# Kernel optimization log

Measured on AMD Instinct MI355X. Metric: run time of the kernel, lower is better.

The kernel has to match this reference:

```python
import jax, jax.numpy as jnp
import numpy as np

ALPHA = 0.2          # LeakyReLU slope
NEG_BIG = -9e15      # mask value from the torch code
LN_EPS = 1e-5        # torch LayerNorm default eps
GAT_SCALE = 1.0


def _layer_norm(x, g, b):
    mu = x.mean(-1, keepdims=True)
    var = ((x - mu) ** 2).mean(-1, keepdims=True)
    return (x - mu) * jax.lax.rsqrt(var + LN_EPS) * g + b


def _gat_layer(h, adj, W, a, concat):
    # h: [B,N,Fin], adj: [N,N] weighted, W: [Fin,Fout], a: [2*Fout,1]
    Wh = jnp.einsum('bnf,fo->bno', h, W)                 # [B,N,Fout]
    Fo = W.shape[1]
    a_i, a_j = a[:Fo, 0], a[Fo:, 0]
    # e[b,i,j] = leakyrelu(Wh[b,i].a_i + Wh[b,j].a_j)  (== cat([Wh_i,Wh_j]) @ a)
    e = jax.nn.leaky_relu(
        (Wh @ a_i)[:, :, None] + (Wh @ a_j)[:, None, :], ALPHA)  # [B,N,N]
    att = jnp.where(adj[None, :, :] > 0, e, NEG_BIG)
    att = jax.nn.softmax(att, axis=2)
    att = att * adj[None, :, :]
    att = att / (att.sum(axis=2, keepdims=True) + 1e-8)
    h_prime = jnp.einsum('bij,bjo->bio', att, Wh)        # [B,N,Fout]
    return jax.nn.elu(h_prime) if concat else h_prime


def setup_inputs() -> dict:
    B, N, H, ID = 1024, 128, 64, 8
    GIN = 1 + ID  # node_feat_dim = 0
    key = jax.random.key(0)
    ks = jax.random.split(key, 20)
    # sparse weighted adjacency with self-loops
    w = jax.random.uniform(ks[0], (N, N))
    m = (jax.random.uniform(ks[1], (N, N)) < 0.3).astype(jnp.float32)
    adj = w * m + jnp.eye(N, dtype=jnp.float32)
    sc = lambda k, s: jax.random.normal(k, s, jnp.float32) * 0.1
    return {
        'c_values': jax.random.normal(ks[2], (B, N), jnp.float32),
        'adj': adj,
        'agent_emb': sc(ks[3], (N, ID)),
        'W1': sc(ks[4], (GIN, H)), 'a1': sc(ks[5], (2 * H, 1)),
        'W2': sc(ks[6], (H, H)),   'a2': sc(ks[7], (2 * H, 1)),
        'ln1_g': jnp.ones((H,)), 'ln1_b': jnp.zeros((H,)),
        'ln2_g': jnp.ones((H,)), 'ln2_b': jnp.zeros((H,)),
        'head_gat_w': sc(ks[8], (H, 1)), 'head_gat_b': jnp.zeros((1,)),
        'mlp1_w': sc(ks[9], (N, H)),  'mlp1_b': jnp.zeros((H,)),
        'mlp2_w': sc(ks[10], (H, H)), 'mlp2_b': jnp.zeros((H,)),
        'head_mlp_w': sc(ks[11], (H, 1)), 'head_mlp_b': jnp.zeros((1,)),
        'gate1_w': sc(ks[12], (N, H)), 'gate1_b': jnp.zeros((H,)),
        'gate2_w': sc(ks[13], (H, 1)), 'gate2_b': jnp.full((1,), -5.0),
    }


def reference(c_values, adj, agent_emb, W1, a1, W2, a2,
              ln1_g, ln1_b, ln2_g, ln2_b, head_gat_w, head_gat_b,
              mlp1_w, mlp1_b, mlp2_w, mlp2_b, head_mlp_w, head_mlp_b,
              gate1_w, gate1_b, gate2_w, gate2_b):
    B, N = c_values.shape
    # node features: [c_value, agent_id_embedding]
    id_feat = jnp.broadcast_to(agent_emb[None], (B, N, agent_emb.shape[1]))
    x_g = jnp.concatenate([c_values[..., None], id_feat], axis=-1)  # [B,N,9]
    h1 = _gat_layer(x_g, adj, W1, a1, concat=True)
    h1 = _layer_norm(h1, ln1_g, ln1_b)
    h2 = _gat_layer(h1, adj, W2, a2, concat=False)
    h = jax.nn.relu(h2 + h1)
    h = _layer_norm(h, ln2_g, ln2_b)
    q_gat = h.mean(axis=1) @ head_gat_w + head_gat_b                # [B,1]
    x_m = jax.nn.relu(c_values @ mlp1_w + mlp1_b)
    x_m = jax.nn.relu(x_m @ mlp2_w + mlp2_b)
    q_mlp = x_m @ head_mlp_w + head_mlp_b                           # [B,1]
    gate = jax.nn.sigmoid(
        jax.nn.relu(c_values @ gate1_w + gate1_b) @ gate2_w + gate2_b)
    return q_mlp + gate * GAT_SCALE * q_gat
```

## Files before the change

kernel.cpp:

```cpp
#include <hip/hip_runtime.h>

typedef unsigned short u16;
typedef unsigned int u32;
typedef short v8s __attribute__((ext_vector_type(8)));
typedef float v4f __attribute__((ext_vector_type(4)));
typedef float v2f __attribute__((ext_vector_type(2)));

__device__ __forceinline__ float bflo(u32 d){union{u32 i;float f;}u;u.i=d<<16;return u.f;}
__device__ __forceinline__ float bfhi(u32 d){union{u32 i;float f;}u;u.i=d&0xffff0000u;return u.f;}
__device__ __forceinline__ u16 f2bfr(float f){union{float f;u32 i;}u;u.f=f;return (u16)((u.i+0x8000u)>>16);}
__device__ __forceinline__ u32 pk2bf(float a,float b){
    union{float f;u32 i;}ua,ub; ua.f=a; ub.f=b;
    u32 x = ua.i + 0x8000u, y = ub.i + 0x8000u;
    return __builtin_amdgcn_perm(y, x, 0x07060302);
}
__device__ __forceinline__ v8s pack8(const float* w){
    union { uint4 u; v8s v; } c;
    c.u.x = pk2bf(w[0],w[1]); c.u.y = pk2bf(w[2],w[3]);
    c.u.z = pk2bf(w[4],w[5]); c.u.w = pk2bf(w[6],w[7]);
    return c.v;
}

__device__ __forceinline__ void flash_att(
    int wv, int l15, int q4,
    const float* __restrict__ ADJ,
    const float* __restrict__ sEi, const float* __restrict__ sFi,
    const float* __restrict__ sEj, const float* __restrict__ sFj,
    const u16* __restrict__ sWhT,
    v4f acc[2][4], float invD[2])
{
    const int r0 = 16*wv + l15, r1 = r0 + 64;
    const v2f Ei0 = {sEi[r0], sEi[r0]}, Fi0 = {sFi[r0], sFi[r0]};
    const v2f Ei1 = {sEi[r1], sEi[r1]}, Fi1 = {sFi[r1], sFi[r1]};
    v2f D0 = {0.f,0.f}, D1 = {0.f,0.f};
    #pragma unroll
    for (int s = 0; s < 2; ++s)
        #pragma unroll
        for (int ct = 0; ct < 4; ++ct) acc[s][ct] = (v4f){0.f,0.f,0.f,0.f};

    #pragma unroll
    for (int ks = 0; ks < 4; ++ks) {
        const int ko = ks*32 + q4*8;
        const v2f* Ejp = (const v2f*)(sEj + ko);
        const v2f* Fjp = (const v2f*)(sFj + ko);
        const v2f* A0p = (const v2f*)(ADJ + r0*128 + ko);
        const v2f* A1p = (const v2f*)(ADJ + r1*128 + ko);
        union { u32 u[4]; v8s v; } P0, P1;
        #pragma unroll
        for (int p = 0; p < 4; ++p) {
            v2f E = Ejp[p], F = Fjp[p];
            v2f a0 = A0p[p], a1 = A1p[p];
            v2f m0 = __builtin_elementwise_max(Ei0*E, Fi0*F);
            v2f m1 = __builtin_elementwise_max(Ei1*E, Fi1*F);
            v2f x0 = m0 * a0;
            v2f x1 = m1 * a1;
            D0 += x0; D1 += x1;
            P0.u[p] = pk2bf(x0.x, x0.y);
            P1.u[p] = pk2bf(x1.x, x1.y);
        }
        #pragma unroll
        for (int ct = 0; ct < 4; ++ct) {
            v8s B = *(const v8s*)(sWhT + (16*ct + l15)*136 + ko);
            acc[0][ct] = __builtin_amdgcn_mfma_f32_16x16x32_bf16(P0.v, B, acc[0][ct], 0,0,0);
            acc[1][ct] = __builtin_amdgcn_mfma_f32_16x16x32_bf16(P1.v, B, acc[1][ct], 0,0,0);
        }
    }
    float d0 = D0.x + D0.y, d1 = D1.x + D1.y;
    d0 += __shfl_xor(d0, 16); d0 += __shfl_xor(d0, 32);
    d1 += __shfl_xor(d1, 16); d1 += __shfl_xor(d1, 32);
    invD[0] = 1.f / d0; invD[1] = 1.f / d1;
}

__global__ __launch_bounds__(256, 4) void graphmixer_kernel(
    const float* __restrict__ C,
    const float* __restrict__ ADJ,
    const float* __restrict__ EMB,
    const float* __restrict__ W1,
    const float* __restrict__ A1,
    const float* __restrict__ W2,
    const float* __restrict__ A2,
    const float* __restrict__ LN1G, const float* __restrict__ LN1B,
    const float* __restrict__ LN2G, const float* __restrict__ LN2B,
    const float* __restrict__ HGW,  const float* __restrict__ HGB,
    const float* __restrict__ MLP1W, const float* __restrict__ MLP1B,
    const float* __restrict__ MLP2W, const float* __restrict__ MLP2B,
    const float* __restrict__ HMW,  const float* __restrict__ HMB,
    const float* __restrict__ G1W,  const float* __restrict__ G1B,
    const float* __restrict__ G2W,  const float* __restrict__ G2B,
    float* __restrict__ OUT)
{
    const int b = blockIdx.x, t = threadIdx.x;
    const int lane = t & 63, wv = t >> 6;
    const int l15 = lane & 15, q4 = lane >> 4;

    __shared__ __align__(16) unsigned char smem[40096];
    u16*   sWhT = (u16*)(smem);
    u16*   sH1  = (u16*)(smem + 17408);
    float* sEi  = (float*)(smem + 35840);
    float* sFi  = (float*)(smem + 36352);
    float* sEj  = (float*)(smem + 36864);
    float* sFj  = (float*)(smem + 37376);
    float* colp = (float*)(smem + 37888);
    float* sScr = (float*)(smem + 38912);
    float* v2i  = (float*)(smem + 39456);
    float* v2j  = (float*)(smem + 39712);
    float* v1i  = (float*)(smem + 39968);
    float* v1j  = (float*)(smem + 40032);
    float* sEmb = (float*)(smem + 17408);
    float* sC   = (float*)(smem + 21504);

    const float* Cb = C + b*128;

    if (wv == 0) {
        #pragma unroll
        for (int q = 0; q < 4; ++q)
            ((float4*)sEmb)[lane + 64*q] = ((const float4*)EMB)[lane + 64*q];
        if (lane < 32) ((float4*)sC)[lane] = ((const float4*)Cb)[lane];
        if (lane >= 32 && lane < 41) {
            int f = lane - 32; float a = 0.f;
            for (int q = 0; q < 16; ++q) {
                float4 w = *(const float4*)(W1 + f*64 + q*4);
                float4 x = *(const float4*)(A1 + q*4);
                a += w.x*x.x + w.y*x.y + w.z*x.z + w.w*x.w;
            }
            v1i[f] = a;
        } else if (lane >= 48 && lane < 57) {
            int f = lane - 48; float a = 0.f;
            for (int q = 0; q < 16; ++q) {
                float4 w = *(const float4*)(W1 + f*64 + q*4);
                float4 x = *(const float4*)(A1 + 64 + q*4);
                a += w.x*x.x + w.y*x.y + w.z*x.z + w.w*x.w;
            }
            v1j[f] = a;
        }
    } else if (wv == 3) {
        float ai = 0.f, aj = 0.f;
        for (int q = 0; q < 16; ++q) {
            float4 w  = *(const float4*)(W2 + lane*64 + q*4);
            float4 xi = *(const float4*)(A2 + q*4);
            float4 xj = *(const float4*)(A2 + 64 + q*4);
            ai += w.x*xi.x + w.y*xi.y + w.z*xi.z + w.w*xi.w;
            aj += w.x*xj.x + w.y*xj.y + w.z*xj.z + w.w*xj.w;
        }
        v2i[lane] = ai; v2j[lane] = aj;
    } else if (wv == 1) {
        float a = 0.f;
        for (int k = 0; k < 128; k += 4) {
            float4 c4 = *(const float4*)(Cb + k);
            a += c4.x*MLP1W[k*64+lane] + c4.y*MLP1W[(k+1)*64+lane]
               + c4.z*MLP1W[(k+2)*64+lane] + c4.w*MLP1W[(k+3)*64+lane];
        }
        sScr[lane] = fmaxf(a + MLP1B[lane], 0.f);
        float a2 = 0.f;
        for (int k = 0; k < 64; ++k) a2 += sScr[k] * MLP2W[k*64 + lane];
        float x2 = fmaxf(a2 + MLP2B[lane], 0.f);
        float p1 = x2 * HMW[lane];
        #pragma unroll
        for (int off = 32; off >= 1; off >>= 1) p1 += __shfl_down(p1, off);
        if (lane == 0) sScr[128] = p1 + HMB[0];
    } else {
        float a = 0.f;
        for (int k = 0; k < 128; k += 4) {
            float4 c4 = *(const float4*)(Cb + k);
            a += c4.x*G1W[k*64+lane] + c4.y*G1W[(k+1)*64+lane]
               + c4.z*G1W[(k+2)*64+lane] + c4.w*G1W[(k+3)*64+lane];
        }
        float g1 = fmaxf(a + G1B[lane], 0.f);
        float p2 = g1 * G2W[lane];
        #pragma unroll
        for (int off = 32; off >= 1; off >>= 1) p2 += __shfl_down(p2, off);
        if (lane == 0) sScr[129] = 1.f / (1.f + __expf(-(p2 + G2B[0])));
    }
    __syncthreads();

    {
        v8s Af[2];
        #pragma unroll
        for (int s = 0; s < 2; ++s) {
            const int row = 16*(wv + 4*s) + l15;
            float av[8];
            #pragma unroll
            for (int j = 0; j < 8; ++j) av[j] = 0.f;
            if (q4 == 0) {
                av[0] = sC[row];
                float4 e0 = *(const float4*)(sEmb + row*8);
                float4 e1 = *(const float4*)(sEmb + row*8 + 4);
                av[1]=e0.x; av[2]=e0.y; av[3]=e0.z; av[4]=e0.w;
                av[5]=e1.x; av[6]=e1.y; av[7]=e1.z;
            } else if (q4 == 1) {
                av[0] = sEmb[row*8 + 7];
            }
            Af[s] = pack8(av);
        }
        #pragma unroll
        for (int ct = 0; ct < 4; ++ct) {
            const int col = 16*ct + l15;
            float bv[8];
            #pragma unroll
            for (int j = 0; j < 8; ++j) bv[j] = 0.f;
            if (q4 == 0) {
                #pragma unroll
                for (int j = 0; j < 8; ++j) bv[j] = W1[j*64 + col];
            } else if (q4 == 1) {
                bv[0] = W1[8*64 + col];
            }
            v8s Bf1 = pack8(bv);
            v4f a0 = (v4f){0.f,0.f,0.f,0.f}, a1 = (v4f){0.f,0.f,0.f,0.f};
            a0 = __builtin_amdgcn_mfma_f32_16x16x32_bf16(Af[0], Bf1, a0, 0,0,0);
            a1 = __builtin_amdgcn_mfma_f32_16x16x32_bf16(Af[1], Bf1, a1, 0,0,0);
            uint2 p0, p1;
            p0.x = pk2bf(a0[0], a0[1]); p0.y = pk2bf(a0[2], a0[3]);
            p1.x = pk2bf(a1[0], a1[1]); p1.y = pk2bf(a1[2], a1[3]);
            *(uint2*)(sWhT + col*136 + 16*wv      + 4*q4) = p0;
            *(uint2*)(sWhT + col*136 + 16*(wv+4)  + 4*q4) = p1;
        }
    }
    {
        const int row = t >> 1;
        const float* vv = (t & 1) ? v1j : v1i;
        float c = sC[row];
        float4 e0 = *(const float4*)(sEmb + row*8);
        float4 e1 = *(const float4*)(sEmb + row*8 + 4);
        float e = c*vv[0] + e0.x*vv[1]+e0.y*vv[2]+e0.z*vv[3]+e0.w*vv[4]
                          + e1.x*vv[5]+e1.y*vv[6]+e1.z*vv[7]+e1.w*vv[8];
        if (t & 1) { sEj[row] = __expf(e); sFj[row] = __expf(0.2f*e); }
        else       { sEi[row] = __expf(e); sFi[row] = __expf(0.2f*e); }
    }
    __syncthreads();

    {
        v4f acc[2][4]; float invD[2];
        flash_att(wv, l15, q4, ADJ, sEi, sFi, sEj, sFj, sWhT, acc, invD);

        float g4[4], b4[4];
        #pragma unroll
        for (int ct = 0; ct < 4; ++ct) { g4[ct] = LN1G[16*ct + l15]; b4[ct] = LN1B[16*ct + l15]; }
        #pragma unroll
        for (int s = 0; s < 2; ++s) {
            const int rbase = 16*(wv + 4*s) + 4*q4;
            #pragma unroll
            for (int reg = 0; reg < 4; ++reg) {
                const int row = rbase + reg;
                const float rd = __shfl(invD[s], 4*q4 + reg);
                float x[4], s1 = 0.f, s2 = 0.f;
                #pragma unroll
                for (int ct = 0; ct < 4; ++ct) {
                    float v = acc[s][ct][reg] * rd;
                    v = (v > 0.f) ? v : (__expf(v) - 1.f);
                    x[ct] = v; s1 += v; s2 += v*v;
                }
                s1 += __shfl_xor(s1, 1); s2 += __shfl_xor(s2, 1);
                s1 += __shfl_xor(s1, 2); s2 += __shfl_xor(s2, 2);
                s1 += __shfl_xor(s1, 4); s2 += __shfl_xor(s2, 4);
                s1 += __shfl_xor(s1, 8); s2 += __shfl_xor(s2, 8);
                const float mean = s1 * (1.f/64.f);
                const float var  = s2 * (1.f/64.f) - mean*mean;
                const float rstd = rsqrtf(var + 1e-5f);
                #pragma unroll
                for (int ct = 0; ct < 4; ++ct) {
                    float h = (x[ct] - mean) * rstd * g4[ct] + b4[ct];
                    sH1[row*72 + 16*ct + l15] = f2bfr(h);
                }
            }
        }
    }

    v8s Bf[2][4];
    #pragma unroll
    for (int ks = 0; ks < 2; ++ks) {
        const int kb = ks*32 + q4*8;
        #pragma unroll
        for (int ct = 0; ct < 4; ++ct) {
            const float* wp = W2 + kb*64 + 16*ct + l15;
            float w8[8];
            #pragma unroll
            for (int j = 0; j < 8; ++j) w8[j] = wp[j*64];
            Bf[ks][ct] = pack8(w8);
        }
    }
    __syncthreads();

    {
        const int row = t >> 1, hb = (t & 1) * 32;
        const u16* hrow = sH1 + row*72 + hb;
        float ei = 0.f, ej = 0.f;
        for (int q = 0; q < 8; ++q) {
            uint2 d = *(const uint2*)(hrow + q*4);
            float h0 = bflo(d.x), h1v = bfhi(d.x), h2 = bflo(d.y), h3 = bfhi(d.y);
            const int kb = hb + q*4;
            ei += h0*v2i[kb+0] + h1v*v2i[kb+1] + h2*v2i[kb+2] + h3*v2i[kb+3];
            ej += h0*v2j[kb+0] + h1v*v2j[kb+1] + h2*v2j[kb+2] + h3*v2j[kb+3];
        }
        ei += __shfl_xor(ei, 1);
        ej += __shfl_xor(ej, 1);
        if ((t & 1) == 0) {
            sEi[row] = __expf(ei); sFi[row] = __expf(0.2f*ei);
            sEj[row] = __expf(ej); sFj[row] = __expf(0.2f*ej);
        }
    }
    {
        v4f acc2[2][4];
        #pragma unroll
        for (int s = 0; s < 2; ++s)
            #pragma unroll
            for (int ct = 0; ct < 4; ++ct) acc2[s][ct] = (v4f){0.f,0.f,0.f,0.f};
        #pragma unroll
        for (int ks = 0; ks < 2; ++ks) {
            const int kb = ks*32 + q4*8;
            #pragma unroll
            for (int s = 0; s < 2; ++s) {
                v8s A = *(const v8s*)(sH1 + (16*(wv+4*s) + l15)*72 + kb);
                #pragma unroll
                for (int ct = 0; ct < 4; ++ct)
                    acc2[s][ct] = __builtin_amdgcn_mfma_f32_16x16x32_bf16(A, Bf[ks][ct], acc2[s][ct], 0,0,0);
            }
        }
        #pragma unroll
        for (int s = 0; s < 2; ++s) {
            const int rb = 16*(wv+4*s) + 4*q4;
            #pragma unroll
            for (int ct = 0; ct < 4; ++ct) {
                const int col = 16*ct + l15;
                uint2 p;
                p.x = pk2bf(acc2[s][ct][0], acc2[s][ct][1]);
                p.y = pk2bf(acc2[s][ct][2], acc2[s][ct][3]);
                *(uint2*)(sWhT + col*136 + rb) = p;
            }
        }
    }
    __syncthreads();

    {
        v4f acc[2][4]; float invD[2];
        flash_att(wv, l15, q4, ADJ, sEi, sFi, sEj, sFj, sWhT, acc, invD);

        float g4[4], b4[4], colsum[4];
        #pragma unroll
        for (int ct = 0; ct < 4; ++ct) {
            g4[ct] = LN2G[16*ct + l15]; b4[ct] = LN2B[16*ct + l15]; colsum[ct] = 0.f;
        }
        #pragma unroll
        for (int s = 0; s < 2; ++s) {
            const int rbase = 16*(wv + 4*s) + 4*q4;
            #pragma unroll
            for (int reg = 0; reg < 4; ++reg) {
                const int row = rbase + reg;
                const float rd = __shfl(invD[s], 4*q4 + reg);
                float x[4], s1 = 0.f, s2 = 0.f;
                #pragma unroll
                for (int ct = 0; ct < 4; ++ct) {
                    float h1v = bflo((u32)sH1[row*72 + 16*ct + l15]);
                    float v = fmaxf(acc[s][ct][reg] * rd + h1v, 0.f);
                    x[ct] = v; s1 += v; s2 += v*v;
                }
                s1 += __shfl_xor(s1, 1); s2 += __shfl_xor(s2, 1);
                s1 += __shfl_xor(s1, 2); s2 += __shfl_xor(s2, 2);
                s1 += __shfl_xor(s1, 4); s2 += __shfl_xor(s2, 4);
                s1 += __shfl_xor(s1, 8); s2 += __shfl_xor(s2, 8);
                const float mean = s1 * (1.f/64.f);
                const float var  = s2 * (1.f/64.f) - mean*mean;
                const float rstd = rsqrtf(var + 1e-5f);
                #pragma unroll
                for (int ct = 0; ct < 4; ++ct)
                    colsum[ct] += (x[ct] - mean) * rstd * g4[ct] + b4[ct];
            }
        }
        #pragma unroll
        for (int ct = 0; ct < 4; ++ct) {
            colsum[ct] += __shfl_xor(colsum[ct], 16);
            colsum[ct] += __shfl_xor(colsum[ct], 32);
        }
        if (lane < 16) {
            #pragma unroll
            for (int ct = 0; ct < 4; ++ct) colp[wv*64 + ct*16 + lane] = colsum[ct];
        }
    }
    __syncthreads();

    if (wv == 0) {
        float s = colp[lane] + colp[64 + lane] + colp[128 + lane] + colp[192 + lane];
        float p = s * (1.f/128.f) * HGW[lane];
        #pragma unroll
        for (int off = 32; off >= 1; off >>= 1) p += __shfl_down(p, off);
        if (lane == 0) OUT[b] = sScr[128] + sScr[129] * (p + HGB[0]);
    }
}

extern "C" void kernel_launch(void* const* d_in, const int* in_sizes, int n_in,
                              void* d_out, int out_size, void* d_ws, size_t ws_size,
                              hipStream_t stream) {
    (void)n_in; (void)out_size; (void)d_ws; (void)ws_size;
    const float* C     = (const float*)d_in[0];
    const float* ADJ   = (const float*)d_in[1];
    const float* EMB   = (const float*)d_in[2];
    const float* W1    = (const float*)d_in[3];
    const float* A1    = (const float*)d_in[4];
    const float* W2    = (const float*)d_in[5];
    const float* A2    = (const float*)d_in[6];
    const float* LN1G  = (const float*)d_in[7];
    const float* LN1B  = (const float*)d_in[8];
    const float* LN2G  = (const float*)d_in[9];
    const float* LN2B  = (const float*)d_in[10];
    const float* HGW   = (const float*)d_in[11];
    const float* HGB   = (const float*)d_in[12];
    const float* MLP1W = (const float*)d_in[13];
    const float* MLP1B = (const float*)d_in[14];
    const float* MLP2W = (const float*)d_in[15];
    const float* MLP2B = (const float*)d_in[16];
    const float* HMW   = (const float*)d_in[17];
    const float* HMB   = (const float*)d_in[18];
    const float* G1W   = (const float*)d_in[19];
    const float* G1B   = (const float*)d_in[20];
    const float* G2W   = (const float*)d_in[21];
    const float* G2B   = (const float*)d_in[22];

    const int B = in_sizes[0] / 128;

    graphmixer_kernel<<<dim3(B), dim3(256), 0, stream>>>(
        C, ADJ, EMB, W1, A1, W2, A2, LN1G, LN1B, LN2G, LN2B,
        HGW, HGB, MLP1W, MLP1B, MLP2W, MLP2B, HMW, HMB,
        G1W, G1B, G2W, G2B, (float*)d_out);
}
```

Baseline: 131.8 us.

## Alias shared buffers to shrink LDS and raise occupancy to five blocks

Shared memory drops from about 40 KB to about 26 KB by putting the WhT and H1 buffers in one region, with extra barriers so one phase finishes before the next overwrites it. Launch bounds ask for 5 blocks per CU. The layer-2 attention logits are now computed inside the LN1 epilogue with shuffle reductions, which removes a separate pass over shared memory. The H1 residual is kept in registers as packed bf16, and the W2 fragments are loaded inside the MFMA loop. The aim is higher occupancy and fewer LDS passes, at the cost of more barriers and more register pressure under the tighter launch bound.

After: 135.4 us. +2.7%, slower.

```diff
diff --git a/kernel.cpp b/kernel.cpp
--- a/kernel.cpp
+++ b/kernel.cpp
@@ -71,7 +71,7 @@
     invD[0] = 1.f / d0; invD[1] = 1.f / d1;
 }
 
-__global__ __launch_bounds__(256, 4) void graphmixer_kernel(
+__global__ __launch_bounds__(256, 5) void graphmixer_kernel(
     const float* __restrict__ C,
     const float* __restrict__ ADJ,
     const float* __restrict__ EMB,
@@ -93,21 +93,20 @@
     const int lane = t & 63, wv = t >> 6;
     const int l15 = lane & 15, q4 = lane >> 4;
 
-    __shared__ __align__(16) unsigned char smem[40096];
-    u16*   sWhT = (u16*)(smem);
-    u16*   sH1  = (u16*)(smem + 17408);
-    float* sEi  = (float*)(smem + 35840);
-    float* sFi  = (float*)(smem + 36352);
-    float* sEj  = (float*)(smem + 36864);
-    float* sFj  = (float*)(smem + 37376);
-    float* colp = (float*)(smem + 37888);
-    float* sScr = (float*)(smem + 38912);
-    float* v2i  = (float*)(smem + 39456);
-    float* v2j  = (float*)(smem + 39712);
-    float* v1i  = (float*)(smem + 39968);
-    float* v1j  = (float*)(smem + 40032);
-    float* sEmb = (float*)(smem + 17408);
-    float* sC   = (float*)(smem + 21504);
+    __shared__ __align__(16) unsigned char smem[26272];
+    u16*   R1   = (u16*)(smem);
+    float* sEi  = (float*)(smem + 18432);
+    float* sFi  = (float*)(smem + 18944);
+    float* sEj  = (float*)(smem + 19456);
+    float* sFj  = (float*)(smem + 19968);
+    float* sScr = (float*)(smem + 20480);
+    float* v2i  = (float*)(smem + 21024);
+    float* v2j  = (float*)(smem + 21280);
+    float* v1i  = (float*)(smem + 21536);
+    float* v1j  = (float*)(smem + 21600);
+    float* sEmb = (float*)(smem + 21664);
+    float* sC   = (float*)(smem + 25760);
+    float* colp = (float*)(smem + 21664);
 
     const float* Cb = C + b*128;
 
@@ -211,8 +210,8 @@
             uint2 p0, p1;
             p0.x = pk2bf(a0[0], a0[1]); p0.y = pk2bf(a0[2], a0[3]);
             p1.x = pk2bf(a1[0], a1[1]); p1.y = pk2bf(a1[2], a1[3]);
-            *(uint2*)(sWhT + col*136 + 16*wv      + 4*q4) = p0;
-            *(uint2*)(sWhT + col*136 + 16*(wv+4)  + 4*q4) = p1;
+            *(uint2*)(R1 + col*136 + 16*wv      + 4*q4) = p0;
+            *(uint2*)(R1 + col*136 + 16*(wv+4)  + 4*q4) = p1;
         }
     }
     {
@@ -228,19 +227,24 @@
     }
     __syncthreads();
 
+    uint2 h1p[2][4];
     {
         v4f acc[2][4]; float invD[2];
-        flash_att(wv, l15, q4, ADJ, sEi, sFi, sEj, sFj, sWhT, acc, invD);
-
-        float g4[4], b4[4];
-        #pragma unroll
-        for (int ct = 0; ct < 4; ++ct) { g4[ct] = LN1G[16*ct + l15]; b4[ct] = LN1B[16*ct + l15]; }
+        flash_att(wv, l15, q4, ADJ, sEi, sFi, sEj, sFj, R1, acc, invD);
+        __syncthreads();
+
+        float g4[4], b4[4], v2i4[4], v2j4[4];
+        #pragma unroll
+        for (int ct = 0; ct < 4; ++ct) {
+            g4[ct] = LN1G[16*ct + l15]; b4[ct] = LN1B[16*ct + l15];
+            v2i4[ct] = v2i[16*ct + l15]; v2j4[ct] = v2j[16*ct + l15];
+        }
         #pragma unroll
         for (int s = 0; s < 2; ++s) {
-            const int rbase = 16*(wv + 4*s) + 4*q4;
+            float hprev[4];
             #pragma unroll
             for (int reg = 0; reg < 4; ++reg) {
-                const int row = rbase + reg;
+                const int ro = 16*(wv + 4*s) + 4*q4 + reg;
                 const float rd = __shfl(invD[s], 4*q4 + reg);
                 float x[4], s1 = 0.f, s2 = 0.f;
                 #pragma unroll
@@ -256,49 +260,38 @@
                 const float mean = s1 * (1.f/64.f);
                 const float var  = s2 * (1.f/64.f) - mean*mean;
                 const float rstd = rsqrtf(var + 1e-5f);
+                float pi = 0.f, pj = 0.f;
                 #pragma unroll
                 for (int ct = 0; ct < 4; ++ct) {
                     float h = (x[ct] - mean) * rstd * g4[ct] + b4[ct];
-                    sH1[row*72 + 16*ct + l15] = f2bfr(h);
+                    R1[ro*72 + 16*ct + l15] = f2bfr(h);
+                    pi += h * v2i4[ct]; pj += h * v2j4[ct];
+                    if ((reg & 1) == 0) hprev[ct] = h;
+                    else if (reg == 1)  h1p[s][ct].x = pk2bf(hprev[ct], h);
+                    else                h1p[s][ct].y = pk2bf(hprev[ct], h);
                 }
-            }
-        }
-    }
-
-    v8s Bf[2][4];
-    #pragma unroll
-    for (int ks = 0; ks < 2; ++ks) {
-        const int kb = ks*32 + q4*8;
-        #pragma unroll
-        for (int ct = 0; ct < 4; ++ct) {
-            const float* wp = W2 + kb*64 + 16*ct + l15;
-            float w8[8];
-            #pragma unroll
-            for (int j = 0; j < 8; ++j) w8[j] = wp[j*64];
-            Bf[ks][ct] = pack8(w8);
+                pi += __shfl_xor(pi, 1); pj += __shfl_xor(pj, 1);
+                pi += __shfl_xor(pi, 2); pj += __shfl_xor(pj, 2);
+                pi += __shfl_xor(pi, 4); pj += __shfl_xor(pj, 4);
+                pi += __shfl_xor(pi, 8); pj += __shfl_xor(pj, 8);
+                if (l15 == 0) {
+                    sEi[ro] = __expf(pi); sFi[ro] = __expf(0.2f*pi);
+                    sEj[ro] = __expf(pj); sFj[ro] = __expf(0.2f*pj);
+                }
+            }
         }
     }
     __syncthreads();
 
     {
-        const int row = t >> 1, hb = (t & 1) * 32;
-        const u16* hrow = sH1 + row*72 + hb;
-        float ei = 0.f, ej = 0.f;
-        for (int q = 0; q < 8; ++q) {
-            uint2 d = *(const uint2*)(hrow + q*4);
-            float h0 = bflo(d.x), h1v = bfhi(d.x), h2 = bflo(d.y), h3 = bfhi(d.y);
-            const int kb = hb + q*4;
-            ei += h0*v2i[kb+0] + h1v*v2i[kb+1] + h2*v2i[kb+2] + h3*v2i[kb+3];
-            ej += h0*v2j[kb+0] + h1v*v2j[kb+1] + h2*v2j[kb+2] + h3*v2j[kb+3];
-        }
-        ei += __shfl_xor(ei, 1);
-        ej += __shfl_xor(ej, 1);
-        if ((t & 1) == 0) {
-            sEi[row] = __expf(ei); sFi[row] = __expf(0.2f*ei);
-            sEj[row] = __expf(ej); sFj[row] = __expf(0.2f*ej);
-        }
-    }
-    {
+        v8s Afrag[2][2];
+        #pragma unroll
+        for (int s = 0; s < 2; ++s)
+            #pragma unroll
+            for (int ks = 0; ks < 2; ++ks)
+                Afrag[s][ks] = *(const v8s*)(R1 + (16*(wv+4*s) + l15)*72 + ks*32 + q4*8);
+        __syncthreads();
+
         v4f acc2[2][4];
         #pragma unroll
         for (int s = 0; s < 2; ++s)
@@ -308,11 +301,15 @@
         for (int ks = 0; ks < 2; ++ks) {
             const int kb = ks*32 + q4*8;
             #pragma unroll
-            for (int s = 0; s < 2; ++s) {
-                v8s A = *(const v8s*)(sH1 + (16*(wv+4*s) + l15)*72 + kb);
-                #pragma unroll
-                for (int ct = 0; ct < 4; ++ct)
-                    acc2[s][ct] = __builtin_amdgcn_mfma_f32_16x16x32_bf16(A, Bf[ks][ct], acc2[s][ct], 0,0,0);
+            for (int ct = 0; ct < 4; ++ct) {
+                const float* wp = W2 + kb*64 + 16*ct + l15;
+                float w8[8];
+                #pragma unroll
+                for (int j = 0; j < 8; ++j) w8[j] = wp[j*64];
+                v8s Bf = pack8(w8);
+                #pragma unroll
+                for (int s = 0; s < 2; ++s)
+                    acc2[s][ct] = __builtin_amdgcn_mfma_f32_16x16x32_bf16(Afrag[s][ks], Bf, acc2[s][ct], 0,0,0);
             }
         }
         #pragma unroll
@@ -324,7 +321,7 @@
                 uint2 p;
                 p.x = pk2bf(acc2[s][ct][0], acc2[s][ct][1]);
                 p.y = pk2bf(acc2[s][ct][2], acc2[s][ct][3]);
-                *(uint2*)(sWhT + col*136 + rb) = p;
+                *(uint2*)(R1 + col*136 + rb) = p;
             }
         }
     }
@@ -332,7 +329,7 @@
 
     {
         v4f acc[2][4]; float invD[2];
-        flash_att(wv, l15, q4, ADJ, sEi, sFi, sEj, sFj, sWhT, acc, invD);
+        flash_att(wv, l15, q4, ADJ, sEi, sFi, sEj, sFj, R1, acc, invD);
 
         float g4[4], b4[4], colsum[4];
         #pragma unroll
@@ -341,15 +338,14 @@
         }
         #pragma unroll
         for (int s = 0; s < 2; ++s) {
-            const int rbase = 16*(wv + 4*s) + 4*q4;
             #pragma unroll
             for (int reg = 0; reg < 4; ++reg) {
-                const int row = rbase + reg;
                 const float rd = __shfl(invD[s], 4*q4 + reg);
                 float x[4], s1 = 0.f, s2 = 0.f;
                 #pragma unroll
                 for (int ct = 0; ct < 4; ++ct) {
-                    float h1v = bflo((u32)sH1[row*72 + 16*ct + l15]);
+                    u32 w = (reg < 2) ? h1p[s][ct].x : h1p[s][ct].y;
+                    float h1v = (reg & 1) ? bfhi(w) : bflo(w);
                     float v = fmaxf(acc[s][ct][reg] * rd + h1v, 0.f);
                     x[ct] = v; s1 += v; s2 += v*v;
                 }
```
